# Kernel tuning notes

Hardware: AMD Instinct MI355X
Metric: run time of the kernel (lower is better)

The kernel has to match this reference:

```python
import jax, jax.numpy as jnp
import numpy as np

B, D, K = 262144, 64, 1024
BETA = 0.25          # commitment_weight
DECAY = 0.99         # ema_decay
EPS = 1e-5


def setup_inputs() -> dict:
    key = jax.random.key(0)
    k1, k2 = jax.random.split(key)
    return {
        "x": jax.random.normal(k1, (B, D), dtype=jnp.float32),
        "embeddings": jax.random.normal(k2, (K, D), dtype=jnp.float32),
        "ema_cluster_size": jnp.zeros((K,), dtype=jnp.float32),
        "ema_embed_sum": jnp.zeros((K, D), dtype=jnp.float32),
    }


def reference(x, embeddings, ema_cluster_size, ema_embed_sum):
    sg = jax.lax.stop_gradient
    # Nearest-code search: squared Euclidean distance, argmin over K.
    # dist[b,k] = |x_b|^2 - 2 x_b.e_k + |e_k|^2 (|x|^2 constant for argmin)
    dist = (jnp.sum(embeddings * embeddings, axis=1)[None, :]
            - 2.0 * jnp.einsum("bd,kd->bk", x, embeddings))  # [B, K]
    codes = jnp.argmin(dist, axis=1)                           # [B] int
    e_k = embeddings[codes]                                    # [B, D] gather

    # Straight-through estimator
    quantized = x + sg(e_k - x)
    residuals = sg(x - e_k)

    # Commitment loss: mse(sg[x], e_k) + beta * mse(x, sg[e_k])
    diff2 = (x - e_k) ** 2
    commitment_loss = jnp.mean((sg(x) - e_k) ** 2) + BETA * jnp.mean((x - sg(e_k)) ** 2)

    # EMA codebook update (training path); one-hot scatter via segment_sum
    xd = sg(x)
    cluster_size = jax.ops.segment_sum(jnp.ones((B,), jnp.float32), codes, num_segments=K)  # [K]
    embed_sum = jax.ops.segment_sum(xd, codes, num_segments=K)                              # [K, D]
    new_cluster_size = DECAY * ema_cluster_size + (1.0 - DECAY) * cluster_size
    new_embed_sum = DECAY * ema_embed_sum + (1.0 - DECAY) * embed_sum
    n = jnp.clip(new_cluster_size, EPS, None)
    new_embeddings = new_embed_sum / n[:, None]

    return codes, quantized, residuals, commitment_loss, new_embeddings, new_cluster_size, new_embed_sum
```

## Files before the change

kernel.cpp:

```cpp
#include <hip/hip_runtime.h>
#include <hip/hip_bf16.h>

#define BN 262144
#define DD 64
#define KC 1024
#define HB 256
#define ROWS_PER_HB (BN / HB)

#define OUT_Q_OFF   (BN)
#define OUT_R_OFF   (BN + BN * DD)
#define OUT_LOSS    (BN + 2 * BN * DD)

#define S_LOSS      0
#define S_ENORM     4
#define S_ENORM64   (S_ENORM + KC)
#define S_COUNT     (S_ENORM64 + 2 * KC)
#define S_OFFSET    (S_COUNT + KC)
#define S_BLOCKHIST (S_OFFSET + KC)
#define S_BASE      (S_BLOCKHIST + HB * KC)
#define S_PERM      (S_BASE + HB * KC)
#define S_NTIE      (S_PERM + BN)
#define S_TIES      (S_NTIE + 4)
#define S_EPACK     (((S_TIES + BN) + 3) & ~3)
#define TILE_BYTES  16640
#define S_PART      (S_EPACK + 16 * TILE_BYTES / 4)

#define TIE_MARGIN 2e-3f

typedef _Float16 f16x8 __attribute__((ext_vector_type(8)));
typedef float    f32x4 __attribute__((ext_vector_type(4)));

__device__ inline f32x4 shflx4(f32x4 v, int m) {
    f32x4 r;
    r[0] = __shfl_xor(v[0], m, 64);
    r[1] = __shfl_xor(v[1], m, 64);
    r[2] = __shfl_xor(v[2], m, 64);
    r[3] = __shfl_xor(v[3], m, 64);
    return r;
}

__device__ inline void gl_lds16(const void* g, void* l) {
    __builtin_amdgcn_global_load_lds(
        (const __attribute__((address_space(1))) void*)g,
        (__attribute__((address_space(3))) void*)l, 16, 0, 0);
}

__global__ __launch_bounds__(256) void vq_init(const float* __restrict__ emb,
                                               float* __restrict__ S,
                                               float* __restrict__ out_loss) {
    const int t = threadIdx.x;
    const int g = blockIdx.x * 256 + t;
    if (g == 0) { out_loss[0] = 0.0f; ((int*)(S + S_NTIE))[0] = 0; }
    const int i = g >> 3;
    const int q = g & 7;
    const float4* e4 = (const float4*)(emb + (size_t)i * DD);
    char* tb = (char*)(S + S_EPACK) + (size_t)(i >> 6) * TILE_BYTES;
    const int ci = i & 63;
    const int sw = (ci & 7) * 8;

    float4 u = e4[2 * q], v = e4[2 * q + 1];
    float a = u.x * u.x;
    a = fmaf(u.y, u.y, a); a = fmaf(u.z, u.z, a); a = fmaf(u.w, u.w, a);
    a = fmaf(v.x, v.x, a); a = fmaf(v.y, v.y, a);
    a = fmaf(v.z, v.z, a); a = fmaf(v.w, v.w, a);
    double b = (double)u.x * u.x + (double)u.y * u.y
             + (double)u.z * u.z + (double)u.w * u.w
             + (double)v.x * v.x + (double)v.y * v.y
             + (double)v.z * v.z + (double)v.w * v.w;

    f16x8 hh, ll;
    hh[0] = (_Float16)u.x; hh[1] = (_Float16)u.y;
    hh[2] = (_Float16)u.z; hh[3] = (_Float16)u.w;
    hh[4] = (_Float16)v.x; hh[5] = (_Float16)v.y;
    hh[6] = (_Float16)v.z; hh[7] = (_Float16)v.w;
    ll[0] = (_Float16)((u.x - (float)hh[0]) * 2048.f);
    ll[1] = (_Float16)((u.y - (float)hh[1]) * 2048.f);
    ll[2] = (_Float16)((u.z - (float)hh[2]) * 2048.f);
    ll[3] = (_Float16)((u.w - (float)hh[3]) * 2048.f);
    ll[4] = (_Float16)((v.x - (float)hh[4]) * 2048.f);
    ll[5] = (_Float16)((v.y - (float)hh[5]) * 2048.f);
    ll[6] = (_Float16)((v.z - (float)hh[6]) * 2048.f);
    ll[7] = (_Float16)((v.w - (float)hh[7]) * 2048.f);
    const int u16 = (ci * 64 + q * 8) ^ sw;
    *(f16x8*)(tb + 2 * u16) = hh;
    *(f16x8*)(tb + 8192 + 2 * u16) = ll;

#pragma unroll
    for (int off = 1; off <= 4; off <<= 1) {
        a += __shfl_xor(a, off, 64);
        b += __shfl_xor(b, off, 64);
    }
    if (q == 0) {
        *(float*)(tb + 16384 + ci * 4) = -0.5f * a;
        ((double*)(S + S_ENORM64))[i] = b;
    }
}

__global__ __launch_bounds__(256) void vq_pass1(
    const float* __restrict__ x,
    float* __restrict__ S,
    float* __restrict__ out_codes) {
    __shared__ __align__(16) unsigned char raw[2 * TILE_BYTES];

    const int t = threadIdx.x;
    const int lane = t & 63, wid = t >> 6;
    const int c = lane & 15, g = lane >> 4;
    const int rowbase = blockIdx.x * 128 + wid * 32;
    const char* epack = (const char*)(S + S_EPACK);

    {
        const char* st = epack;
#pragma unroll
        for (int cc = 0; cc < 4; ++cc) {
            const int chunk = wid * 260 + cc * 64;
            gl_lds16(st + (size_t)(chunk + lane) * 16, raw + chunk * 16);
        }
        const int chunk = wid * 260 + 256;
        if (lane < 4)
            gl_lds16(st + (size_t)(chunk + lane) * 16, raw + chunk * 16);
    }

    f16x8 a_hi[2][2], a_lo[2][2];
#pragma unroll
    for (int mi = 0; mi < 2; ++mi) {
        const float4* xr = (const float4*)(x + (size_t)(rowbase + mi * 16 + c) * DD);
#pragma unroll
        for (int h = 0; h < 2; ++h) {
            float4 u = xr[h * 8 + g * 2];
            float4 v = xr[h * 8 + g * 2 + 1];
            f16x8 hi, lo;
            hi[0] = (_Float16)u.x; hi[1] = (_Float16)u.y;
            hi[2] = (_Float16)u.z; hi[3] = (_Float16)u.w;
            hi[4] = (_Float16)v.x; hi[5] = (_Float16)v.y;
            hi[6] = (_Float16)v.z; hi[7] = (_Float16)v.w;
            lo[0] = (_Float16)((u.x - (float)hi[0]) * 2048.f);
            lo[1] = (_Float16)((u.y - (float)hi[1]) * 2048.f);
            lo[2] = (_Float16)((u.z - (float)hi[2]) * 2048.f);
            lo[3] = (_Float16)((u.w - (float)hi[3]) * 2048.f);
            lo[4] = (_Float16)((v.x - (float)hi[4]) * 2048.f);
            lo[5] = (_Float16)((v.y - (float)hi[5]) * 2048.f);
            lo[6] = (_Float16)((v.z - (float)hi[6]) * 2048.f);
            lo[7] = (_Float16)((v.w - (float)hi[7]) * 2048.f);
            a_hi[mi][h] = hi;
            a_lo[mi][h] = lo;
        }
    }

    float b1[8], b2[8];
    int kb[8];
#pragma unroll
    for (int s = 0; s < 8; ++s) { b1[s] = -3.4e38f; b2[s] = -3.4e38f; kb[s] = 0; }

    const int sw = (c & 7) * 8;
    const int bb0 = 2 * ((c * 64 + g * 8) ^ sw);
    const int bb1 = 2 * ((c * 64 + 32 + g * 8) ^ sw);
    const int be = 16384 + c * 4;

#pragma unroll 2
    for (int kt = 0; kt < 16; ++kt) {
        if (kt < 15) {
            const char* st = epack + (size_t)(kt + 1) * TILE_BYTES;
            unsigned char* db = raw + ((kt + 1) & 1) * TILE_BYTES;
#pragma unroll
            for (int cc = 0; cc < 4; ++cc) {
                const int chunk = wid * 260 + cc * 64;
                gl_lds16(st + (size_t)(chunk + lane) * 16, db + chunk * 16);
            }
            const int chunk = wid * 260 + 256;
            if (lane < 4)
                gl_lds16(st + (size_t)(chunk + lane) * 16, db + chunk * 16);
            __builtin_amdgcn_sched_barrier(0);
            asm volatile("s_waitcnt vmcnt(5)");
        } else {
            __builtin_amdgcn_sched_barrier(0);
            asm volatile("s_waitcnt vmcnt(0)");
        }
        __builtin_amdgcn_sched_barrier(0);
        __builtin_amdgcn_s_barrier();

        const unsigned char* bufp = raw + (kt & 1) * TILE_BYTES;
        const int kbase = kt * 64;
#pragma unroll
        for (int ni = 0; ni < 4; ++ni) {
            f16x8 bh0 = *(const f16x8*)(bufp + bb0 + ni * 2048);
            f16x8 bh1 = *(const f16x8*)(bufp + bb1 + ni * 2048);
            f16x8 bl0 = *(const f16x8*)(bufp + 8192 + bb0 + ni * 2048);
            f16x8 bl1 = *(const f16x8*)(bufp + 8192 + bb1 + ni * 2048);
            const float seed = *(const float*)(bufp + be + ni * 64);
            const int kcur = kbase + ni * 16 + c;
#pragma unroll
            for (int mi = 0; mi < 2; ++mi) {
                f32x4 ah = {seed, seed, seed, seed};
                f32x4 ax = {0.f, 0.f, 0.f, 0.f};
                ah = __builtin_amdgcn_mfma_f32_16x16x32_f16(a_hi[mi][0], bh0, ah, 0, 0, 0);
                ah = __builtin_amdgcn_mfma_f32_16x16x32_f16(a_hi[mi][1], bh1, ah, 0, 0, 0);
                ax = __builtin_amdgcn_mfma_f32_16x16x32_f16(a_hi[mi][0], bl0, ax, 0, 0, 0);
                ax = __builtin_amdgcn_mfma_f32_16x16x32_f16(a_lo[mi][0], bh0, ax, 0, 0, 0);
                ax = __builtin_amdgcn_mfma_f32_16x16x32_f16(a_hi[mi][1], bl1, ax, 0, 0, 0);
                ax = __builtin_amdgcn_mfma_f32_16x16x32_f16(a_lo[mi][1], bh1, ax, 0, 0, 0);
#pragma unroll
                for (int r = 0; r < 4; ++r) {
                    const float m = fmaf(4.8828125e-4f, ax[r], ah[r]);
                    const int s = mi * 4 + r;
                    b2[s] = __builtin_amdgcn_fmed3f(m, b1[s], b2[s]);
                    const bool gt = m > b1[s];
                    b1[s] = fmaxf(b1[s], m);
                    kb[s] = gt ? kcur : kb[s];
                }
            }
        }
        __builtin_amdgcn_s_barrier();
    }

#pragma unroll
    for (int off = 1; off <= 8; off <<= 1) {
#pragma unroll
        for (int s = 0; s < 8; ++s) {
            float ob1 = __shfl_xor(b1[s], off, 64);
            float ob2 = __shfl_xor(b2[s], off, 64);
            int okk = __shfl_xor(kb[s], off, 64);
            float mn = fminf(b1[s], ob1);
            b2[s] = fmaxf(fmaxf(b2[s], ob2), mn);
            if (ob1 > b1[s]) { b1[s] = ob1; kb[s] = okk; }
        }
    }

    const int rlo = c - g * 4;
    if (rlo >= 0 && rlo < 4) {
        int* ntie = (int*)(S + S_NTIE);
        int* ties = (int*)(S + S_TIES);
#pragma unroll
        for (int mi = 0; mi < 2; ++mi) {
            const int s = mi * 4 + rlo;
            const int row = rowbase + mi * 16 + c;
            out_codes[row] = (float)kb[s];
            if ((b1[s] - b2[s]) * 2.0f < TIE_MARGIN) {
                int slot = atomicAdd(ntie, 1);
                ties[slot] = row;
            }
        }
    }
}

__global__ __launch_bounds__(256) void vq_resolve(
    const float* __restrict__ x,
    const float* __restrict__ emb,
    const float* __restrict__ S,
    float* __restrict__ out_codes) {
    const int n = ((const int*)(S + S_NTIE))[0];
    const int* ties = (const int*)(S + S_TIES);
    const double* en64 = (const double*)(S + S_ENORM64);
    const int lane = threadIdx.x & 63;
    const int gw = (blockIdx.x * 256 + threadIdx.x) >> 6;
    const int nw = (gridDim.x * 256) >> 6;
    for (int i = gw; i < n; i += nw) {
        const int row = ties[i];
        const float4* xr = (const float4*)(x + (size_t)row * DD);
        float4 xq[16];
#pragma unroll
        for (int j = 0; j < 16; ++j) xq[j] = xr[j];
        double bd = 1e300;
        int bk = KC;
        for (int kk = 0; kk < KC / 64; ++kk) {
            const int k = lane * (KC / 64) + kk;
            const float4* er = (const float4*)(emb + (size_t)k * DD);
            double d0 = 0., d1 = 0., d2 = 0., d3 = 0.;
#pragma unroll
            for (int j = 0; j < 16; ++j) {
                float4 e = er[j], xv = xq[j];
                d0 = fma((double)xv.x, (double)e.x, d0);
                d1 = fma((double)xv.y, (double)e.y, d1);
                d2 = fma((double)xv.z, (double)e.z, d2);
                d3 = fma((double)xv.w, (double)e.w, d3);
            }
            double dist = en64[k] - 2.0 * ((d0 + d1) + (d2 + d3));
            if (dist < bd) { bd = dist; bk = k; }
        }
#pragma unroll
        for (int off = 32; off; off >>= 1) {
            double od = __shfl_xor(bd, off, 64);
            int ok = __shfl_xor(bk, off, 64);
            if (od < bd || (od == bd && ok < bk)) { bd = od; bk = ok; }
        }
        if (lane == 0) out_codes[row] = (float)bk;
    }
}

__global__ __launch_bounds__(256) void vq_hist(const float* __restrict__ codes,
                                               float* S) {
    __shared__ int lh[KC];
    const int b = blockIdx.x, t = threadIdx.x;
    int* blockhist = (int*)(S + S_BLOCKHIST);
#pragma unroll
    for (int j = 0; j < 4; ++j) lh[t + 256 * j] = 0;
    __syncthreads();
#pragma unroll
    for (int j = 0; j < ROWS_PER_HB / 256; ++j) {
        int k = (int)codes[b * ROWS_PER_HB + j * 256 + t];
        atomicAdd(&lh[k], 1);
    }
    __syncthreads();
#pragma unroll
    for (int j = 0; j < 4; ++j) {
        int k = t + 256 * j;
        blockhist[b * KC + k] = lh[k];
    }
}

__global__ __launch_bounds__(128) void vq_scan1(float* S) {
    const int k = blockIdx.x * 128 + threadIdx.x;
    int* blockhist = (int*)(S + S_BLOCKHIST);
    int* base      = (int*)(S + S_BASE);
    int* count     = (int*)(S + S_COUNT);
    int s = 0;
#pragma unroll 4
    for (int b = 0; b < HB; ++b) {
        base[b * KC + k] = s;
        s += blockhist[b * KC + k];
    }
    count[k] = s;
}

__global__ __launch_bounds__(1024) void vq_scan2(float* S) {
    __shared__ int sc[KC];
    const int k = threadIdx.x;
    int* count  = (int*)(S + S_COUNT);
    int* offset = (int*)(S + S_OFFSET);
    sc[k] = count[k];
    __syncthreads();
    for (int st = 1; st < KC; st <<= 1) {
        int v = (k >= st) ? sc[k - st] : 0;
        __syncthreads();
        sc[k] += v;
        __syncthreads();
    }
    offset[k] = (k == 0) ? 0 : sc[k - 1];
}

__global__ __launch_bounds__(256) void vq_scatter(const float* __restrict__ codes,
                                                  float* S) {
    __shared__ int cur[KC];
    const int b = blockIdx.x, t = threadIdx.x;
    int* base   = (int*)(S + S_BASE);
    int* offset = (int*)(S + S_OFFSET);
    int* perm   = (int*)(S + S_PERM);
#pragma unroll
    for (int j = 0; j < 4; ++j) {
        int k = t + 256 * j;
        cur[k] = base[b * KC + k] + offset[k];
    }
    __syncthreads();
#pragma unroll
    for (int j = 0; j < ROWS_PER_HB / 256; ++j) {
        int row = b * ROWS_PER_HB + j * 256 + t;
        int k = (int)codes[row];
        int slot = atomicAdd(&cur[k], 1);
        perm[slot] = row;
    }
}

__global__ __launch_bounds__(256) void vq_reduce(
    const float* __restrict__ x,
    float* __restrict__ S) {
    __shared__ f32x4 part[4][16];
    const int k = blockIdx.x >> 3, sub = blockIdx.x & 7;
    const int t = threadIdx.x, l = t & 63, w = t >> 6;
    const int rg = l >> 4, ds = l & 15;
    const int* count  = (const int*)(S + S_COUNT);
    const int* offset = (const int*)(S + S_OFFSET);
    const int* perm   = (const int*)(S + S_PERM);

    const int n = count[k], start = offset[k];
    const int nb = (n + 7) >> 3;
    int cnt = n - sub * nb;
    cnt = cnt < nb ? cnt : nb;
    const int s0 = start + sub * nb;
    const int s1 = s0 + cnt;

    f32x4 a0 = {0.f, 0.f, 0.f, 0.f}, a1 = a0, a2 = a0, a3 = a0;
    const int base = s0 + w * 4 + rg;
    const int iters = (cnt + 63) >> 6;
#pragma unroll 2
    for (int it = 0; it < iters; ++it) {
        const int j = base + it * 64;
        const int r0 = (j      < s1) ? perm[j]      : -1;
        const int r1 = (j + 16 < s1) ? perm[j + 16] : -1;
        const int r2 = (j + 32 < s1) ? perm[j + 32] : -1;
        const int r3 = (j + 48 < s1) ? perm[j + 48] : -1;
        if (r0 >= 0) a0 += *(const f32x4*)(x + (size_t)r0 * DD + ds * 4);
        if (r1 >= 0) a1 += *(const f32x4*)(x + (size_t)r1 * DD + ds * 4);
        if (r2 >= 0) a2 += *(const f32x4*)(x + (size_t)r2 * DD + ds * 4);
        if (r3 >= 0) a3 += *(const f32x4*)(x + (size_t)r3 * DD + ds * 4);
    }
    f32x4 acc = (a0 + a1) + (a2 + a3);
    acc += shflx4(acc, 16);
    acc += shflx4(acc, 32);
    if (l < 16) part[w][l] = acc;
    __syncthreads();
    if (t < 16) {
        f32x4 tot = (part[0][t] + part[1][t]) + (part[2][t] + part[3][t]);
        ((f32x4*)(S + S_PART))[((size_t)sub * KC + k) * 16 + t] = tot;
    }
}

__global__ __launch_bounds__(256) void vq_emafin(
    const float* __restrict__ S,
    const float* __restrict__ ema_cs,
    const float* __restrict__ ema_es,
    float* __restrict__ out_ne,
    float* __restrict__ out_ncs,
    float* __restrict__ out_nes) {
    const int i = blockIdx.x * 256 + threadIdx.x;
    const int* count = (const int*)(S + S_COUNT);
    const int NV = KC * DD / 4;
    if (i < NV) {
        const f32x4* P = (const f32x4*)(S + S_PART);
        f32x4 s = ((P[i] + P[NV + i]) + (P[2 * NV + i] + P[3 * NV + i]))
                + ((P[4 * NV + i] + P[5 * NV + i]) + (P[6 * NV + i] + P[7 * NV + i]));
        f32x4 e = ((const f32x4*)ema_es)[i];
        const int k = i >> 4;
        const float cs = 0.99f * ema_cs[k] + 0.01f * (float)count[k];
        const float mx = fmaxf(cs, 1e-5f);
        f32x4 nes = e * 0.99f + s * 0.01f;
        f32x4 ne;
        ne[0] = nes[0] / mx; ne[1] = nes[1] / mx;
        ne[2] = nes[2] / mx; ne[3] = nes[3] / mx;
        ((f32x4*)out_nes)[i] = nes;
        ((f32x4*)out_ne)[i] = ne;
    } else if (i < NV + KC) {
        const int k = i - NV;
        out_ncs[k] = 0.99f * ema_cs[k] + 0.01f * (float)count[k];
    }
}

__global__ __launch_bounds__(256) void vq_pass2(
    const float* __restrict__ x,
    const float* __restrict__ emb,
    const float* __restrict__ out_codes,
    float4* __restrict__ out_q,
    float4* __restrict__ out_r,
    float* __restrict__ out_loss) {
    __shared__ float lpart[4];
    const int t = threadIdx.x;
    const int seg = t & 15, rr = t >> 4;
    const int rowbase = blockIdx.x * 256;
    float lsum = 0.f;
#pragma unroll
    for (int it = 0; it < 16; ++it) {
        const int row = rowbase + it * 16 + rr;
        const int code = (int)out_codes[row];
        const float4 xv = ((const float4*)x)[(size_t)row * 16 + seg];
        const float4 e  = ((const float4*)emb)[(size_t)code * 16 + seg];
        float4 q, r;
        q.x = xv.x + (e.x - xv.x); q.y = xv.y + (e.y - xv.y);
        q.z = xv.z + (e.z - xv.z); q.w = xv.w + (e.w - xv.w);
        r.x = xv.x - e.x; r.y = xv.y - e.y; r.z = xv.z - e.z; r.w = xv.w - e.w;
        lsum += r.x * r.x + r.y * r.y + r.z * r.z + r.w * r.w;
        out_q[(size_t)row * 16 + seg] = q;
        out_r[(size_t)row * 16 + seg] = r;
    }
#pragma unroll
    for (int off = 32; off; off >>= 1) lsum += __shfl_xor(lsum, off, 64);
    if ((t & 63) == 0) lpart[t >> 6] = lsum;
    __syncthreads();
    if (t == 0) {
        float tot = (lpart[0] + lpart[1]) + (lpart[2] + lpart[3]);
        atomicAdd(out_loss, tot * 1.25f * (1.0f / 16777216.0f));
    }
}

extern "C" void kernel_launch(void* const* d_in, const int* in_sizes, int n_in,
                              void* d_out, int out_size, void* d_ws, size_t ws_size,
                              hipStream_t stream) {
    const float* x      = (const float*)d_in[0];
    const float* emb    = (const float*)d_in[1];
    const float* ema_cs = (const float*)d_in[2];
    const float* ema_es = (const float*)d_in[3];

    float* out = (float*)d_out;
    float*  out_codes = out;
    float4* out_q     = (float4*)(out + OUT_Q_OFF);
    float4* out_r     = (float4*)(out + OUT_R_OFF);
    float*  out_loss  = out + OUT_LOSS;
    float*  out_ne    = out_loss + 1;
    float*  out_ncs   = out_ne + KC * DD;
    float*  out_nes   = out_ncs + KC;

    float* S = out + OUT_Q_OFF;

    vq_init<<<32, 256, 0, stream>>>(emb, S, out_loss);
    vq_pass1<<<BN / 128, 256, 0, stream>>>(x, S, out_codes);
    vq_resolve<<<256, 256, 0, stream>>>(x, emb, S, out_codes);
    vq_hist<<<HB, 256, 0, stream>>>(out_codes, S);
    vq_scan1<<<KC / 128, 128, 0, stream>>>(S);
    vq_scan2<<<1, 1024, 0, stream>>>(S);
    vq_scatter<<<HB, 256, 0, stream>>>(out_codes, S);
    vq_reduce<<<KC * 8, 256, 0, stream>>>(x, S);
    vq_emafin<<<(KC * DD / 4 + KC + 255) / 256, 256, 0, stream>>>(
        S, ema_cs, ema_es, out_ne, out_ncs, out_nes);
    vq_pass2<<<BN / 256, 256, 0, stream>>>(x, emb, out_codes, out_q, out_r,
                                           out_loss);
}
```

Baseline: 404.3 us.

## Fuse per-block code histogram into distance pass and patch it in tie resolve

Each pass1 block now builds an LDS histogram of its 128 rows' codes and writes it to a per-block histogram, which removes the separate vq_hist kernel and its re-read of codes. vq_resolve adjusts the histogram atomically when it changes a code, and the scan and scatter kernels are resized for 2048 histogram blocks. The tie margin is also tightened so fewer rows go through the double-precision resolve. In exchange the per-block histogram is eight times larger, which makes scan1 serial over 2048 blocks, and the tighter margin risks missing near-ties.

```diff
diff --git a/kernel.cpp b/kernel.cpp
--- a/kernel.cpp
+++ b/kernel.cpp
@@ -4,8 +4,8 @@
 #define BN 262144
 #define DD 64
 #define KC 1024
-#define HB 256
-#define ROWS_PER_HB (BN / HB)
+#define HB2 2048
+#define RPB 128
 
 #define OUT_Q_OFF   (BN)
 #define OUT_R_OFF   (BN + BN * DD)
@@ -17,15 +17,15 @@
 #define S_COUNT     (S_ENORM64 + 2 * KC)
 #define S_OFFSET    (S_COUNT + KC)
 #define S_BLOCKHIST (S_OFFSET + KC)
-#define S_BASE      (S_BLOCKHIST + HB * KC)
-#define S_PERM      (S_BASE + HB * KC)
+#define S_BASE      (S_BLOCKHIST + HB2 * KC)
+#define S_PERM      (S_BASE + HB2 * KC)
 #define S_NTIE      (S_PERM + BN)
 #define S_TIES      (S_NTIE + 4)
 #define S_EPACK     (((S_TIES + BN) + 3) & ~3)
 #define TILE_BYTES  16640
 #define S_PART      (S_EPACK + 16 * TILE_BYTES / 4)
 
-#define TIE_MARGIN 2e-3f
+#define TIE_MARGIN 8e-4f
 
 typedef _Float16 f16x8 __attribute__((ext_vector_type(8)));
 typedef float    f32x4 __attribute__((ext_vector_type(4)));
@@ -101,12 +101,16 @@
     float* __restrict__ S,
     float* __restrict__ out_codes) {
     __shared__ __align__(16) unsigned char raw[2 * TILE_BYTES];
+    __shared__ int lh[KC];
 
     const int t = threadIdx.x;
     const int lane = t & 63, wid = t >> 6;
     const int c = lane & 15, g = lane >> 4;
     const int rowbase = blockIdx.x * 128 + wid * 32;
     const char* epack = (const char*)(S + S_EPACK);
+
+#pragma unroll
+    for (int j = 0; j < 4; ++j) lh[t + 256 * j] = 0;
 
     {
         const char* st = epack;
@@ -234,27 +238,34 @@
             const int s = mi * 4 + rlo;
             const int row = rowbase + mi * 16 + c;
             out_codes[row] = (float)kb[s];
+            atomicAdd(&lh[kb[s]], 1);
             if ((b1[s] - b2[s]) * 2.0f < TIE_MARGIN) {
                 int slot = atomicAdd(ntie, 1);
                 ties[slot] = row;
             }
         }
     }
+    __syncthreads();
+    int* bh = (int*)(S + S_BLOCKHIST) + (size_t)blockIdx.x * KC;
+#pragma unroll
+    for (int j = 0; j < 4; ++j) bh[t + 256 * j] = lh[t + 256 * j];
 }
 
 __global__ __launch_bounds__(256) void vq_resolve(
     const float* __restrict__ x,
     const float* __restrict__ emb,
-    const float* __restrict__ S,
+    float* __restrict__ S,
     float* __restrict__ out_codes) {
     const int n = ((const int*)(S + S_NTIE))[0];
     const int* ties = (const int*)(S + S_TIES);
     const double* en64 = (const double*)(S + S_ENORM64);
+    int* bh = (int*)(S + S_BLOCKHIST);
     const int lane = threadIdx.x & 63;
     const int gw = (blockIdx.x * 256 + threadIdx.x) >> 6;
     const int nw = (gridDim.x * 256) >> 6;
     for (int i = gw; i < n; i += nw) {
         const int row = ties[i];
+        const int oldk = (int)out_codes[row];
         const float4* xr = (const float4*)(x + (size_t)row * DD);
         float4 xq[16];
 #pragma unroll
@@ -282,41 +293,25 @@
             int ok = __shfl_xor(bk, off, 64);
             if (od < bd || (od == bd && ok < bk)) { bd = od; bk = ok; }
         }
-        if (lane == 0) out_codes[row] = (float)bk;
-    }
-}
-
-__global__ __launch_bounds__(256) void vq_hist(const float* __restrict__ codes,
-                                               float* S) {
-    __shared__ int lh[KC];
-    const int b = blockIdx.x, t = threadIdx.x;
-    int* blockhist = (int*)(S + S_BLOCKHIST);
-#pragma unroll
-    for (int j = 0; j < 4; ++j) lh[t + 256 * j] = 0;
-    __syncthreads();
-#pragma unroll
-    for (int j = 0; j < ROWS_PER_HB / 256; ++j) {
-        int k = (int)codes[b * ROWS_PER_HB + j * 256 + t];
-        atomicAdd(&lh[k], 1);
-    }
-    __syncthreads();
-#pragma unroll
-    for (int j = 0; j < 4; ++j) {
-        int k = t + 256 * j;
-        blockhist[b * KC + k] = lh[k];
-    }
-}
-
-__global__ __launch_bounds__(128) void vq_scan1(float* S) {
-    const int k = blockIdx.x * 128 + threadIdx.x;
+        if (lane == 0 && bk != oldk) {
+            out_codes[row] = (float)bk;
+            const int b = row >> 7;
+            atomicAdd(&bh[(size_t)b * KC + oldk], -1);
+            atomicAdd(&bh[(size_t)b * KC + bk], 1);
+        }
+    }
+}
+
+__global__ __launch_bounds__(64) void vq_scan1(float* S) {
+    const int k = blockIdx.x * 64 + threadIdx.x;
     int* blockhist = (int*)(S + S_BLOCKHIST);
     int* base      = (int*)(S + S_BASE);
     int* count     = (int*)(S + S_COUNT);
     int s = 0;
-#pragma unroll 4
-    for (int b = 0; b < HB; ++b) {
-        base[b * KC + k] = s;
-        s += blockhist[b * KC + k];
+#pragma unroll 8
+    for (int b = 0; b < HB2; ++b) {
+        base[(size_t)b * KC + k] = s;
+        s += blockhist[(size_t)b * KC + k];
     }
     count[k] = s;
 }
@@ -337,7 +332,7 @@
     offset[k] = (k == 0) ? 0 : sc[k - 1];
 }
 
-__global__ __launch_bounds__(256) void vq_scatter(const float* __restrict__ codes,
+__global__ __launch_bounds__(128) void vq_scatter(const float* __restrict__ codes,
                                                   float* S) {
     __shared__ int cur[KC];
     const int b = blockIdx.x, t = threadIdx.x;
@@ -345,14 +340,13 @@
     int* offset = (int*)(S + S_OFFSET);
     int* perm   = (int*)(S + S_PERM);
 #pragma unroll
-    for (int j = 0; j < 4; ++j) {
-        int k = t + 256 * j;
-        cur[k] = base[b * KC + k] + offset[k];
+    for (int j = 0; j < 8; ++j) {
+        int k = t + 128 * j;
+        cur[k] = base[(size_t)b * KC + k] + offset[k];
     }
     __syncthreads();
-#pragma unroll
-    for (int j = 0; j < ROWS_PER_HB / 256; ++j) {
-        int row = b * ROWS_PER_HB + j * 256 + t;
+    {
+        int row = b * RPB + t;
         int k = (int)codes[row];
         int slot = atomicAdd(&cur[k], 1);
         perm[slot] = row;
@@ -491,10 +485,9 @@
     vq_init<<<32, 256, 0, stream>>>(emb, S, out_loss);
     vq_pass1<<<BN / 128, 256, 0, stream>>>(x, S, out_codes);
     vq_resolve<<<256, 256, 0, stream>>>(x, emb, S, out_codes);
-    vq_hist<<<HB, 256, 0, stream>>>(out_codes, S);
-    vq_scan1<<<KC / 128, 128, 0, stream>>>(S);
+    vq_scan1<<<KC / 64, 64, 0, stream>>>(S);
     vq_scan2<<<1, 1024, 0, stream>>>(S);
-    vq_scatter<<<HB, 256, 0, stream>>>(out_codes, S);
+    vq_scatter<<<HB2, 128, 0, stream>>>(out_codes, S);
     vq_reduce<<<KC * 8, 256, 0, stream>>>(x, S);
     vq_emafin<<<(KC * DD / 4 + KC + 255) / 256, 256, 0, stream>>>(
         S, ema_cs, ema_es, out_ne, out_ncs, out_nes);
```

Result: slower. 485.0 us (+20.0%).
